# Performance work log

Measured on AMD Instinct MI355X. Metric: run time of the kernel, lower is better.

The kernel has to match this reference:

```python
import jax, jax.numpy as jnp
import numpy as np

NUM_HEADS = 8
NORM_GROUPS = 32
EPS = 1e-5


def setup_inputs() -> dict:
    key = jax.random.key(0)
    k1, k2, k3 = jax.random.split(key, 3)
    b, c, h, w = 16, 256, 64, 64
    x = jax.random.normal(k1, (b, c, h, w), dtype=jnp.float32)
    gn_w = jnp.ones((c,), dtype=jnp.float32)
    gn_b = jnp.zeros((c,), dtype=jnp.float32)
    # 1x1 convs == channel matmuls; init like torch (kaiming-ish scale)
    w_qkv = jax.random.normal(k2, (3 * c, c), dtype=jnp.float32) / np.sqrt(c)
    w_proj = jax.random.normal(k3, (c, c), dtype=jnp.float32) / np.sqrt(c)
    b_proj = jnp.zeros((c,), dtype=jnp.float32)
    return {"x": x, "gn_w": gn_w, "gn_b": gn_b, "w_qkv": w_qkv,
            "w_proj": w_proj, "b_proj": b_proj}


def reference(x, gn_w, gn_b, w_qkv, w_proj, b_proj):
    b, c, h, w = x.shape
    H = NUM_HEADS
    d = c // H
    n = h * w
    # GroupNorm over (channels_per_group, h, w)
    xg = x.reshape(b, NORM_GROUPS, -1)
    mu = jnp.mean(xg, axis=-1, keepdims=True)
    var = jnp.mean(jnp.square(xg - mu), axis=-1, keepdims=True)
    xn = ((xg - mu) * jax.lax.rsqrt(var + EPS)).reshape(b, c, h, w)
    xn = xn * gn_w[None, :, None, None] + gn_b[None, :, None, None]
    # 1x1 conv -> (b, 3c, h, w); channel layout is (qkv, heads, d)
    qkv = jnp.einsum('oc,bchw->bohw', w_qkv, xn)
    qkv = qkv.reshape(b, 3, H, d, n)
    q, k, v = qkv[:, 0], qkv[:, 1], qkv[:, 2]  # each (b, H, d, n)
    k = jax.nn.softmax(k, axis=-1)
    # linear attention: small (d x d) state per head
    att = jnp.einsum('bhdn,bhen->bhde', k, v)
    out = jnp.einsum('bhde,bhdn->bhen', att, q)  # (b, H, d, n)
    out = out.reshape(b, c, h, w)
    return jnp.einsum('oc,bchw->bohw', w_proj, out) + b_proj[None, :, None, None]
```

## Files before the change

kernel.cpp:

```cpp
#include <hip/hip_runtime.h>
#include <stdint.h>

#define BATCH 16
#define CCH   256
#define NSP   4096
#define QKV_M 768

typedef unsigned short u16;
typedef short  short8 __attribute__((ext_vector_type(8)));
typedef float  f32x4  __attribute__((ext_vector_type(4)));

__device__ __forceinline__ float bf2f(u16 h) {
  union { unsigned int u; float f; } x; x.u = ((unsigned int)h) << 16; return x.f;
}
__device__ __forceinline__ u16 f2bf(float f) {
  union { float f; unsigned int u; } x; x.f = f;
  unsigned int r = 0x7fffu + ((x.u >> 16) & 1u);
  return (u16)((x.u + r) >> 16);
}

#define GLB(p) ((__attribute__((address_space(1))) void*)(p))
#define LDSP(p) ((__attribute__((address_space(3))) void*)(p))

__global__ __launch_bounds__(256) void convw_kernel(const float* __restrict__ wq,
                                                    const float* __restrict__ wp,
                                                    u16* __restrict__ dst) {
  const int i = (blockIdx.x * 256 + threadIdx.x) * 4;
  float4 v = (i < 196608) ? *(const float4*)(wq + i)
                          : *(const float4*)(wp + (i - 196608));
  ushort4 o;
  o.x = f2bf(v.x); o.y = f2bf(v.y); o.z = f2bf(v.z); o.w = f2bf(v.w);
  *(ushort4*)(dst + i) = o;
}

__global__ __launch_bounds__(256) void gn_stats(const float* __restrict__ x,
                                                float2* __restrict__ stats,
                                                float* __restrict__ att4) {
  const int blk = blockIdx.x;
  const int tid = threadIdx.x;
  {
    float* az = att4 + (size_t)blk * 264;
    for (int i = tid; i < 264; i += 256) az[i] = 0.f;
  }
  const float4* xv = (const float4*)(x + (size_t)blk * 32768);
  float s = 0.f, ss = 0.f;
  for (int i = tid; i < 8192; i += 256) {
    float4 u = xv[i];
    s  += u.x + u.y + u.z + u.w;
    ss += u.x * u.x + u.y * u.y + u.z * u.z + u.w * u.w;
  }
#pragma unroll
  for (int off = 32; off > 0; off >>= 1) {
    s  += __shfl_down(s, off);
    ss += __shfl_down(ss, off);
  }
  __shared__ float red[8];
  const int wave = tid >> 6, lane = tid & 63;
  if (lane == 0) { red[wave * 2] = s; red[wave * 2 + 1] = ss; }
  __syncthreads();
  if (tid == 0) {
    const float S  = red[0] + red[2] + red[4] + red[6];
    const float SS = red[1] + red[3] + red[5] + red[7];
    const float mean = S * (1.f / 32768.f);
    const float var  = SS * (1.f / 32768.f) - mean * mean;
    stats[blk] = make_float2(mean, rsqrtf(var + 1e-5f));
  }
}

__global__ __launch_bounds__(256) void gn_apply_t(const float* __restrict__ x,
                                                  const float* __restrict__ gw,
                                                  const float* __restrict__ gb,
                                                  const float2* __restrict__ stats,
                                                  u16* __restrict__ xnT) {
  __shared__ u16 ls[64][72];
  const int b = blockIdx.z, c0 = blockIdx.y * 64, n0 = blockIdx.x * 64;
  const int tid = threadIdx.x;
#pragma unroll
  for (int r = 0; r < 4; ++r) {
    const int cc = (tid >> 4) + r * 16;
    const int nn = (tid & 15) * 4;
    const int c = c0 + cc;
    const float2 st = stats[b * 32 + (c >> 3)];
    const float wv = gw[c] * st.y;
    const float bv = gb[c] - st.x * wv;
    float4 u = *(const float4*)(x + ((size_t)b * CCH + c) * NSP + n0 + nn);
    ushort4 o;
    o.x = f2bf(u.x * wv + bv);
    o.y = f2bf(u.y * wv + bv);
    o.z = f2bf(u.z * wv + bv);
    o.w = f2bf(u.w * wv + bv);
    *(ushort4*)&ls[cc][nn] = o;
  }
  __syncthreads();
#pragma unroll
  for (int p = 0; p < 2; ++p) {
    const int idx = tid + p * 256;
    const int nn = idx >> 3;
    const int cb = (idx & 7) * 8;
    u16 tmp[8];
#pragma unroll
    for (int j = 0; j < 8; ++j) tmp[j] = ls[cb + j][nn];
    *(uint4*)(xnT + ((size_t)b * NSP + n0 + nn) * CCH + c0 + cb) = *(uint4*)tmp;
  }
}

template <int OUTF32, int TRQ>
__global__ __launch_bounds__(256) void gemm_mfma(const u16* __restrict__ A,
                                                 const u16* __restrict__ Bt,
                                                 const float* __restrict__ bias,
                                                 void* __restrict__ Cm, int M,
                                                 int aBatch, long btStride) {
  __shared__ __align__(16) u16 smem[17408];
  const int tid = threadIdx.x, wave = tid >> 6, lane = tid & 63;
  const int n0 = blockIdx.x * 128, m0 = blockIdx.y * 128, bz = blockIdx.z;
  const u16* Ab = A + (size_t)bz * aBatch;
  const u16* Bb = Bt + (size_t)bz * btStride;

  const int lrow = lane >> 3;
  const int kcl  = ((lane & 7) ^ lrow) * 8;
  const u16* pA[4]; const u16* pB[4];
#pragma unroll
  for (int j = 0; j < 4; ++j) {
    const int row = j * 32 + wave * 8 + lrow;
    pA[j] = Ab + (size_t)(m0 + row) * CCH + kcl;
    pB[j] = Bb + (size_t)(n0 + row) * CCH + kcl;
  }
  u16* lA = smem;
  u16* lB = smem + 8192;

  const int wm = wave >> 1, wn = wave & 1;
  f32x4 acc[4][4];
#pragma unroll
  for (int i = 0; i < 4; ++i)
#pragma unroll
    for (int j = 0; j < 4; ++j) acc[i][j] = (f32x4){0.f, 0.f, 0.f, 0.f};

  for (int it = 0; it < 4; ++it) {
#pragma unroll
    for (int j = 0; j < 4; ++j) {
      __builtin_amdgcn_global_load_lds(GLB(pA[j]), LDSP(lA + (j * 256 + wave * 64) * 8), 16, 0, 0);
      __builtin_amdgcn_global_load_lds(GLB(pB[j]), LDSP(lB + (j * 256 + wave * 64) * 8), 16, 0, 0);
      pA[j] += 64; pB[j] += 64;
    }
    __syncthreads();
#pragma unroll
    for (int w = 0; w < 2; ++w) {
      const int kcf = w * 4 + (lane >> 4);
      short8 af[4], bfr[4];
#pragma unroll
      for (int mt = 0; mt < 4; ++mt) {
        const int row = wm * 64 + mt * 16 + (lane & 15);
        af[mt] = *(const short8*)&lA[(row * 8 + (kcf ^ (row & 7))) * 8];
      }
#pragma unroll
      for (int nt = 0; nt < 4; ++nt) {
        const int row = wn * 64 + nt * 16 + (lane & 15);
        bfr[nt] = *(const short8*)&lB[(row * 8 + (kcf ^ (row & 7))) * 8];
      }
#pragma unroll
      for (int mt = 0; mt < 4; ++mt)
#pragma unroll
        for (int nt = 0; nt < 4; ++nt)
          acc[mt][nt] = __builtin_amdgcn_mfma_f32_16x16x32_bf16(af[mt], bfr[nt], acc[mt][nt], 0, 0, 0);
    }
    __syncthreads();
  }

  if (!OUTF32) {
    u16* cl = smem;
    const bool tr = TRQ && (m0 < 256);
#pragma unroll
    for (int mt = 0; mt < 4; ++mt)
#pragma unroll
      for (int nt = 0; nt < 4; ++nt)
#pragma unroll
        for (int r = 0; r < 4; ++r) {
          const int row = wm * 64 + mt * 16 + (lane >> 4) * 4 + r;
          const int col = wn * 64 + nt * 16 + (lane & 15);
          if (tr) cl[col * 136 + row] = f2bf(acc[mt][nt][r]);
          else    cl[row * 136 + col] = f2bf(acc[mt][nt][r]);
        }
    __syncthreads();
    u16* C = (u16*)Cm + (size_t)bz * M * NSP;
    if (tr) {
#pragma unroll
      for (int j = 0; j < 8; ++j) {
        const int idx = tid + j * 256;
        const int nl = idx >> 4, mc = (idx & 15) * 8;
        *(uint4*)(C + (size_t)(n0 + nl) * CCH + m0 + mc) =
            *(const uint4*)&cl[nl * 136 + mc];
      }
    } else {
#pragma unroll
      for (int j = 0; j < 8; ++j) {
        const int idx = tid + j * 256;
        const int row = idx >> 4, chunk = idx & 15;
        *(uint4*)(C + (size_t)(m0 + row) * NSP + n0 + chunk * 8) =
            *(const uint4*)&cl[row * 136 + chunk * 8];
      }
    }
  } else {
    float* clf = (float*)smem;
    float* C = (float*)Cm + (size_t)bz * M * NSP;
#pragma unroll
    for (int pass = 0; pass < 2; ++pass) {
      if (wm == pass) {
#pragma unroll
        for (int mt = 0; mt < 4; ++mt)
#pragma unroll
          for (int nt = 0; nt < 4; ++nt)
#pragma unroll
            for (int r = 0; r < 4; ++r) {
              const int rl = mt * 16 + (lane >> 4) * 4 + r;
              const int col = wn * 64 + nt * 16 + (lane & 15);
              clf[rl * 132 + col] = acc[mt][nt][r] + bias[m0 + pass * 64 + rl];
            }
      }
      __syncthreads();
#pragma unroll
      for (int j = 0; j < 8; ++j) {
        const int idx = tid + j * 256;
        const int row = idx >> 5, chunk = idx & 31;
        *(float4*)(C + (size_t)(m0 + pass * 64 + row) * NSP + n0 + chunk * 4) =
            *(const float4*)&clf[row * 132 + chunk * 4];
      }
      __syncthreads();
    }
  }
}

__global__ __launch_bounds__(256) void gemm_kv_att(const u16* __restrict__ A,
                                                   const u16* __restrict__ Bt,
                                                   float* __restrict__ att4) {
  __shared__ __align__(16) u16 smem[34816];
  const int tid = threadIdx.x, wave = tid >> 6, lane = tid & 63;
  const int n0 = blockIdx.x * 128, hg = blockIdx.y, b = blockIdx.z;
  const u16* Bb = Bt + (size_t)b * (size_t)NSP * CCH;

  const int lrow = lane >> 3;
  const int kcl  = ((lane & 7) ^ lrow) * 8;
  u16* lA  = smem;
  u16* lB  = smem + 8192;
  u16* clK = smem + 17408;
  u16* clV = smem;
  const int wm = wave >> 1, wn = wave & 1;

  for (int pass = 0; pass < 2; ++pass) {
    const int m0 = 256 + pass * 256 + hg * 128;
    const u16* pA[4]; const u16* pB[4];
#pragma unroll
    for (int j = 0; j < 4; ++j) {
      const int row = j * 32 + wave * 8 + lrow;
      pA[j] = A  + (size_t)(m0 + row) * CCH + kcl;
      pB[j] = Bb + (size_t)(n0 + row) * CCH + kcl;
    }
    f32x4 acc[4][4];
#pragma unroll
    for (int i = 0; i < 4; ++i)
#pragma unroll
      for (int j = 0; j < 4; ++j) acc[i][j] = (f32x4){0.f, 0.f, 0.f, 0.f};

    for (int it = 0; it < 4; ++it) {
#pragma unroll
      for (int j = 0; j < 4; ++j) {
        __builtin_amdgcn_global_load_lds(GLB(pA[j]), LDSP(lA + (j * 256 + wave * 64) * 8), 16, 0, 0);
        __builtin_amdgcn_global_load_lds(GLB(pB[j]), LDSP(lB + (j * 256 + wave * 64) * 8), 16, 0, 0);
        pA[j] += 64; pB[j] += 64;
      }
      __syncthreads();
#pragma unroll
      for (int w = 0; w < 2; ++w) {
        const int kcf = w * 4 + (lane >> 4);
        short8 af[4], bfr[4];
#pragma unroll
        for (int mt = 0; mt < 4; ++mt) {
          const int row = wm * 64 + mt * 16 + (lane & 15);
          af[mt] = *(const short8*)&lA[(row * 8 + (kcf ^ (row & 7))) * 8];
        }
#pragma unroll
        for (int nt = 0; nt < 4; ++nt) {
          const int row = wn * 64 + nt * 16 + (lane & 15);
          bfr[nt] = *(const short8*)&lB[(row * 8 + (kcf ^ (row & 7))) * 8];
        }
#pragma unroll
        for (int mt = 0; mt < 4; ++mt)
#pragma unroll
          for (int nt = 0; nt < 4; ++nt)
            acc[mt][nt] = __builtin_amdgcn_mfma_f32_16x16x32_bf16(af[mt], bfr[nt], acc[mt][nt], 0, 0, 0);
      }
      __syncthreads();
    }

    u16* cl = pass ? clV : clK;
#pragma unroll
    for (int mt = 0; mt < 4; ++mt)
#pragma unroll
      for (int nt = 0; nt < 4; ++nt)
#pragma unroll
        for (int r = 0; r < 4; ++r) {
          const int row = wm * 64 + mt * 16 + (lane >> 4) * 4 + r;
          const int col = wn * 64 + nt * 16 + (lane & 15);
          const float v = acc[mt][nt][r];
          cl[row * 136 + col] = f2bf(pass ? v : __expf(v));
        }
  }
  __syncthreads();

  const int hh = wave;
  const int bh = b * 8 + hg * 4 + hh;
  f32x4 a2[2][2], al[2];
#pragma unroll
  for (int i = 0; i < 2; ++i) {
    al[i] = (f32x4){0.f, 0.f, 0.f, 0.f};
#pragma unroll
    for (int j = 0; j < 2; ++j) a2[i][j] = (f32x4){0.f, 0.f, 0.f, 0.f};
  }
  short8 ones;
#pragma unroll
  for (int j = 0; j < 8; ++j) ones[j] = (short)0x3F80;

  const int rr = lane & 15, cc8 = (lane >> 4) * 8;
#pragma unroll
  for (int c = 0; c < 4; ++c) {
    const int n = c * 32 + cc8;
    short8 ek0 = *(const short8*)&clK[(hh * 32 + rr) * 136 + n];
    short8 ek1 = *(const short8*)&clK[(hh * 32 + 16 + rr) * 136 + n];
    short8 v0  = *(const short8*)&clV[(hh * 32 + rr) * 136 + n];
    short8 v1  = *(const short8*)&clV[(hh * 32 + 16 + rr) * 136 + n];
    a2[0][0] = __builtin_amdgcn_mfma_f32_16x16x32_bf16(ek0, v0, a2[0][0], 0, 0, 0);
    a2[0][1] = __builtin_amdgcn_mfma_f32_16x16x32_bf16(ek0, v1, a2[0][1], 0, 0, 0);
    a2[1][0] = __builtin_amdgcn_mfma_f32_16x16x32_bf16(ek1, v0, a2[1][0], 0, 0, 0);
    a2[1][1] = __builtin_amdgcn_mfma_f32_16x16x32_bf16(ek1, v1, a2[1][1], 0, 0, 0);
    al[0]    = __builtin_amdgcn_mfma_f32_16x16x32_bf16(ek0, ones, al[0], 0, 0, 0);
    al[1]    = __builtin_amdgcn_mfma_f32_16x16x32_bf16(ek1, ones, al[1], 0, 0, 0);
  }

  float* ap = att4 + (size_t)bh * 1056;
  const int dq = (lane >> 4) * 4;
#pragma unroll
  for (int dh = 0; dh < 2; ++dh) {
#pragma unroll
    for (int eh = 0; eh < 2; ++eh)
#pragma unroll
      for (int j = 0; j < 4; ++j)
        atomicAdd(&ap[(dh * 16 + dq + j) * 32 + eh * 16 + rr], a2[dh][eh][j]);
    if (rr == 0)
#pragma unroll
      for (int j = 0; j < 4; ++j)
        atomicAdd(&ap[1024 + dh * 16 + dq + j], al[dh][j]);
  }
}

__global__ __launch_bounds__(256) void w2_kernel(const u16* __restrict__ wp_bf,
                                                 const float* __restrict__ att4,
                                                 u16* __restrict__ W2) {
  const int b = blockIdx.x >> 4;
  const int o0 = (blockIdx.x & 15) * 16;
  const int tid = threadIdx.x;
  const int h = tid >> 5, d = tid & 31;
  const float* ap = att4 + ((size_t)b * 8 + h) * 1056;
  const float linv = 1.f / ap[1024 + d];
  float as[32];
#pragma unroll
  for (int e = 0; e < 32; ++e) as[e] = ap[d * 32 + e] * linv;
  u16* w2p = W2 + (size_t)b * 65536;
  for (int oi = 0; oi < 16; ++oi) {
    const int o = o0 + oi;
    const uint4* wr = (const uint4*)(wp_bf + o * 256 + h * 32);
    float acc = 0.f;
#pragma unroll
    for (int j = 0; j < 4; ++j) {
      uint4 u = wr[j];
      const u16* w8 = (const u16*)&u;
#pragma unroll
      for (int t = 0; t < 8; ++t) acc += bf2f(w8[t]) * as[j * 8 + t];
    }
    w2p[o * 256 + tid] = f2bf(acc);
  }
}

extern "C" void kernel_launch(void* const* d_in, const int* in_sizes, int n_in,
                              void* d_out, int out_size, void* d_ws, size_t ws_size,
                              hipStream_t stream) {
  const float* x      = (const float*)d_in[0];
  const float* gn_w   = (const float*)d_in[1];
  const float* gn_b   = (const float*)d_in[2];
  const float* w_qkv  = (const float*)d_in[3];
  const float* w_proj = (const float*)d_in[4];
  const float* b_proj = (const float*)d_in[5];
  float* out = (float*)d_out;

  char* ws = (char*)d_ws;
  u16*    xnT   = (u16*)ws;
  u16*    qkv   = (u16*)(ws + 33554432ull);
  float*  att4  = (float*)(ws + 134217728ull);
  float2* stats = (float2*)(ws + 134758400ull);
  u16*    wbf   = (u16*)(ws + 134762496ull);
  u16* wq_bf = wbf;
  u16* wp_bf = wbf + 196608;
  u16* W2 = xnT;

  convw_kernel<<<256, 256, 0, stream>>>(w_qkv, w_proj, wbf);
  gn_stats<<<512, 256, 0, stream>>>(x, stats, att4);
  gn_apply_t<<<dim3(64, 4, 16), 256, 0, stream>>>(x, gn_w, gn_b, stats, xnT);
  gemm_mfma<0, 1><<<dim3(32, 2, 16), 256, 0, stream>>>(wq_bf, xnT, nullptr, qkv,
                                                       QKV_M, 0, (long)NSP * CCH);
  gemm_kv_att<<<dim3(32, 2, 16), 256, 0, stream>>>(wq_bf, xnT, att4);
  w2_kernel<<<256, 256, 0, stream>>>(wp_bf, att4, W2);
  gemm_mfma<1, 0><<<dim3(32, 2, 16), 256, 0, stream>>>(W2, qkv, b_proj, out,
                                                       CCH, 65536, (long)QKV_M * NSP);
}
```

Baseline: 246.9 us.

## Fold query projection into output weights and drop QKV materialization

```diff
diff --git a/kernel.cpp b/kernel.cpp
--- a/kernel.cpp
+++ b/kernel.cpp
@@ -4,7 +4,6 @@
 #define BATCH 16
 #define CCH   256
 #define NSP   4096
-#define QKV_M 768
 
 typedef unsigned short u16;
 typedef short  short8 __attribute__((ext_vector_type(8)));
@@ -31,6 +30,27 @@
   ushort4 o;
   o.x = f2bf(v.x); o.y = f2bf(v.y); o.z = f2bf(v.z); o.w = f2bf(v.w);
   *(ushort4*)(dst + i) = o;
+}
+
+__global__ __launch_bounds__(256) void wqt_kernel(const u16* __restrict__ wq_bf,
+                                                  u16* __restrict__ wqT) {
+  __shared__ u16 ls[64][72];
+  const int r0 = blockIdx.y * 64, c0 = blockIdx.x * 64;
+  const int t = threadIdx.x;
+#pragma unroll
+  for (int j = 0; j < 2; ++j) {
+    const int row = j * 32 + (t >> 3), col8 = (t & 7) * 8;
+    *(uint4*)&ls[row][col8] = *(const uint4*)(wq_bf + (r0 + row) * 256 + c0 + col8);
+  }
+  __syncthreads();
+#pragma unroll
+  for (int j = 0; j < 2; ++j) {
+    const int crow = j * 32 + (t >> 3), d8 = (t & 7) * 8;
+    u16 tmp[8];
+#pragma unroll
+    for (int k = 0; k < 8; ++k) tmp[k] = ls[d8 + k][crow];
+    *(uint4*)(wqT + (c0 + crow) * 256 + r0 + d8) = *(uint4*)tmp;
+  }
 }
 
 __global__ __launch_bounds__(256) void gn_stats(const float* __restrict__ x,
@@ -104,12 +124,12 @@
   }
 }
 
-template <int OUTF32, int TRQ>
+template <int OUTF32>
 __global__ __launch_bounds__(256) void gemm_mfma(const u16* __restrict__ A,
                                                  const u16* __restrict__ Bt,
                                                  const float* __restrict__ bias,
                                                  void* __restrict__ Cm, int M,
-                                                 int aBatch, long btStride) {
+                                                 int aBatch, long btStride, int ldc) {
   __shared__ __align__(16) u16 smem[17408];
   const int tid = threadIdx.x, wave = tid >> 6, lane = tid & 63;
   const int n0 = blockIdx.x * 128, m0 = blockIdx.y * 128, bz = blockIdx.z;
@@ -168,7 +188,6 @@
 
   if (!OUTF32) {
     u16* cl = smem;
-    const bool tr = TRQ && (m0 < 256);
 #pragma unroll
     for (int mt = 0; mt < 4; ++mt)
 #pragma unroll
@@ -177,31 +196,20 @@
         for (int r = 0; r < 4; ++r) {
           const int row = wm * 64 + mt * 16 + (lane >> 4) * 4 + r;
           const int col = wn * 64 + nt * 16 + (lane & 15);
-          if (tr) cl[col * 136 + row] = f2bf(acc[mt][nt][r]);
-          else    cl[row * 136 + col] = f2bf(acc[mt][nt][r]);
+          cl[row * 136 + col] = f2bf(acc[mt][nt][r]);
         }
     __syncthreads();
-    u16* C = (u16*)Cm + (size_t)bz * M * NSP;
-    if (tr) {
-#pragma unroll
-      for (int j = 0; j < 8; ++j) {
-        const int idx = tid + j * 256;
-        const int nl = idx >> 4, mc = (idx & 15) * 8;
-        *(uint4*)(C + (size_t)(n0 + nl) * CCH + m0 + mc) =
-            *(const uint4*)&cl[nl * 136 + mc];
-      }
-    } else {
-#pragma unroll
-      for (int j = 0; j < 8; ++j) {
-        const int idx = tid + j * 256;
-        const int row = idx >> 4, chunk = idx & 15;
-        *(uint4*)(C + (size_t)(m0 + row) * NSP + n0 + chunk * 8) =
-            *(const uint4*)&cl[row * 136 + chunk * 8];
-      }
+    u16* C = (u16*)Cm + (size_t)bz * (size_t)M * ldc;
+#pragma unroll
+    for (int j = 0; j < 8; ++j) {
+      const int idx = tid + j * 256;
+      const int row = idx >> 4, chunk = idx & 15;
+      *(uint4*)(C + (size_t)(m0 + row) * ldc + n0 + chunk * 8) =
+          *(const uint4*)&cl[row * 136 + chunk * 8];
     }
   } else {
     float* clf = (float*)smem;
-    float* C = (float*)Cm + (size_t)bz * M * NSP;
+    float* C = (float*)Cm + (size_t)bz * (size_t)M * ldc;
 #pragma unroll
     for (int pass = 0; pass < 2; ++pass) {
       if (wm == pass) {
@@ -221,7 +229,7 @@
       for (int j = 0; j < 8; ++j) {
         const int idx = tid + j * 256;
         const int row = idx >> 5, chunk = idx & 31;
-        *(float4*)(C + (size_t)(m0 + pass * 64 + row) * NSP + n0 + chunk * 4) =
+        *(float4*)(C + (size_t)(m0 + pass * 64 + row) * ldc + n0 + chunk * 4) =
             *(const float4*)&clf[row * 132 + chunk * 4];
       }
       __syncthreads();
@@ -232,7 +240,7 @@
 __global__ __launch_bounds__(256) void gemm_kv_att(const u16* __restrict__ A,
                                                    const u16* __restrict__ Bt,
                                                    float* __restrict__ att4) {
-  __shared__ __align__(16) u16 smem[34816];
+  __shared__ __align__(16) u16 smem[20992];
   const int tid = threadIdx.x, wave = tid >> 6, lane = tid & 63;
   const int n0 = blockIdx.x * 128, hg = blockIdx.y, b = blockIdx.z;
   const u16* Bb = Bt + (size_t)b * (size_t)NSP * CCH;
@@ -240,41 +248,46 @@
   const int lrow = lane >> 3;
   const int kcl  = ((lane & 7) ^ lrow) * 8;
   u16* lA  = smem;
-  u16* lB  = smem + 8192;
-  u16* clK = smem + 17408;
+  u16* lB  = smem + 4096;
   u16* clV = smem;
+  u16* clK = smem + 12288;
   const int wm = wave >> 1, wn = wave & 1;
 
   for (int pass = 0; pass < 2; ++pass) {
-    const int m0 = 256 + pass * 256 + hg * 128;
-    const u16* pA[4]; const u16* pB[4];
-#pragma unroll
-    for (int j = 0; j < 4; ++j) {
-      const int row = j * 32 + wave * 8 + lrow;
-      pA[j] = A  + (size_t)(m0 + row) * CCH + kcl;
-      pB[j] = Bb + (size_t)(n0 + row) * CCH + kcl;
-    }
-    f32x4 acc[4][4];
-#pragma unroll
-    for (int i = 0; i < 4; ++i)
+    const int m0 = 256 + pass * 256 + hg * 64;
+    const u16* pA[2]; const u16* pB[4];
+#pragma unroll
+    for (int j = 0; j < 2; ++j)
+      pA[j] = A + (size_t)(m0 + j * 32 + wave * 8 + lrow) * CCH + kcl;
+#pragma unroll
+    for (int j = 0; j < 4; ++j)
+      pB[j] = Bb + (size_t)(n0 + j * 32 + wave * 8 + lrow) * CCH + kcl;
+
+    f32x4 acc[2][4];
+#pragma unroll
+    for (int i = 0; i < 2; ++i)
 #pragma unroll
       for (int j = 0; j < 4; ++j) acc[i][j] = (f32x4){0.f, 0.f, 0.f, 0.f};
 
     for (int it = 0; it < 4; ++it) {
 #pragma unroll
+      for (int j = 0; j < 2; ++j) {
+        __builtin_amdgcn_global_load_lds(GLB(pA[j]), LDSP(lA + (j * 256 + wave * 64) * 8), 16, 0, 0);
+        pA[j] += 64;
+      }
+#pragma unroll
       for (int j = 0; j < 4; ++j) {
-        __builtin_amdgcn_global_load_lds(GLB(pA[j]), LDSP(lA + (j * 256 + wave * 64) * 8), 16, 0, 0);
         __builtin_amdgcn_global_load_lds(GLB(pB[j]), LDSP(lB + (j * 256 + wave * 64) * 8), 16, 0, 0);
-        pA[j] += 64; pB[j] += 64;
+        pB[j] += 64;
       }
       __syncthreads();
 #pragma unroll
       for (int w = 0; w < 2; ++w) {
         const int kcf = w * 4 + (lane >> 4);
-        short8 af[4], bfr[4];
-#pragma unroll
-        for (int mt = 0; mt < 4; ++mt) {
-          const int row = wm * 64 + mt * 16 + (lane & 15);
+        short8 af[2], bfr[4];
+#pragma unroll
+        for (int mt = 0; mt < 2; ++mt) {
+          const int row = wm * 32 + mt * 16 + (lane & 15);
           af[mt] = *(const short8*)&lA[(row * 8 + (kcf ^ (row & 7))) * 8];
         }
 #pragma unroll
@@ -283,7 +296,7 @@
           bfr[nt] = *(const short8*)&lB[(row * 8 + (kcf ^ (row & 7))) * 8];
         }
 #pragma unroll
-        for (int mt = 0; mt < 4; ++mt)
+        for (int mt = 0; mt < 2; ++mt)
 #pragma unroll
           for (int nt = 0; nt < 4; ++nt)
             acc[mt][nt] = __builtin_amdgcn_mfma_f32_16x16x32_bf16(af[mt], bfr[nt], acc[mt][nt], 0, 0, 0);
@@ -293,12 +306,12 @@
 
     u16* cl = pass ? clV : clK;
 #pragma unroll
-    for (int mt = 0; mt < 4; ++mt)
+    for (int mt = 0; mt < 2; ++mt)
 #pragma unroll
       for (int nt = 0; nt < 4; ++nt)
 #pragma unroll
         for (int r = 0; r < 4; ++r) {
-          const int row = wm * 64 + mt * 16 + (lane >> 4) * 4 + r;
+          const int row = wm * 32 + mt * 16 + (lane >> 4) * 4 + r;
           const int col = wn * 64 + nt * 16 + (lane & 15);
           const float v = acc[mt][nt][r];
           cl[row * 136 + col] = f2bf(pass ? v : __expf(v));
@@ -306,8 +319,8 @@
   }
   __syncthreads();
 
-  const int hh = wave;
-  const int bh = b * 8 + hg * 4 + hh;
+  const int hh = wave >> 1, nhalf = wave & 1;
+  const int bh = b * 8 + hg * 2 + hh;
   f32x4 a2[2][2], al[2];
 #pragma unroll
   for (int i = 0; i < 2; ++i) {
@@ -321,8 +334,8 @@
 
   const int rr = lane & 15, cc8 = (lane >> 4) * 8;
 #pragma unroll
-  for (int c = 0; c < 4; ++c) {
-    const int n = c * 32 + cc8;
+  for (int c = 0; c < 2; ++c) {
+    const int n = (nhalf * 2 + c) * 32 + cc8;
     short8 ek0 = *(const short8*)&clK[(hh * 32 + rr) * 136 + n];
     short8 ek1 = *(const short8*)&clK[(hh * 32 + 16 + rr) * 136 + n];
     short8 v0  = *(const short8*)&clV[(hh * 32 + rr) * 136 + n];
@@ -334,20 +347,43 @@
     al[0]    = __builtin_amdgcn_mfma_f32_16x16x32_bf16(ek0, ones, al[0], 0, 0, 0);
     al[1]    = __builtin_amdgcn_mfma_f32_16x16x32_bf16(ek1, ones, al[1], 0, 0, 0);
   }
-
-  float* ap = att4 + (size_t)bh * 1056;
+  __syncthreads();
+
+  float* red  = (float*)smem;
+  float* redl = red + 2176;
   const int dq = (lane >> 4) * 4;
-#pragma unroll
-  for (int dh = 0; dh < 2; ++dh) {
-#pragma unroll
-    for (int eh = 0; eh < 2; ++eh)
-#pragma unroll
-      for (int j = 0; j < 4; ++j)
-        atomicAdd(&ap[(dh * 16 + dq + j) * 32 + eh * 16 + rr], a2[dh][eh][j]);
-    if (rr == 0)
-#pragma unroll
-      for (int j = 0; j < 4; ++j)
-        atomicAdd(&ap[1024 + dh * 16 + dq + j], al[dh][j]);
+  if (nhalf == 1) {
+#pragma unroll
+    for (int dh = 0; dh < 2; ++dh) {
+#pragma unroll
+      for (int eh = 0; eh < 2; ++eh)
+#pragma unroll
+        for (int j = 0; j < 4; ++j)
+          red[hh * 1088 + (dh * 16 + dq + j) * 34 + eh * 16 + rr] = a2[dh][eh][j];
+      if (rr == 0)
+#pragma unroll
+        for (int j = 0; j < 4; ++j) redl[hh * 32 + dh * 16 + dq + j] = al[dh][j];
+    }
+  }
+  __syncthreads();
+  if (nhalf == 0) {
+    float* ap = att4 + (size_t)bh * 1056;
+#pragma unroll
+    for (int dh = 0; dh < 2; ++dh) {
+#pragma unroll
+      for (int eh = 0; eh < 2; ++eh)
+#pragma unroll
+        for (int j = 0; j < 4; ++j) {
+          const int d = dh * 16 + dq + j, e = eh * 16 + rr;
+          atomicAdd(&ap[d * 32 + e], a2[dh][eh][j] + red[hh * 1088 + d * 34 + e]);
+        }
+      if (rr == 0)
+#pragma unroll
+        for (int j = 0; j < 4; ++j) {
+          const int d = dh * 16 + dq + j;
+          atomicAdd(&ap[1024 + d], al[dh][j] + redl[hh * 32 + d]);
+        }
+    }
   }
 }
 
@@ -392,21 +428,23 @@
 
   char* ws = (char*)d_ws;
   u16*    xnT   = (u16*)ws;
-  u16*    qkv   = (u16*)(ws + 33554432ull);
-  float*  att4  = (float*)(ws + 134217728ull);
-  float2* stats = (float2*)(ws + 134758400ull);
-  u16*    wbf   = (u16*)(ws + 134762496ull);
+  u16*    wbf   = (u16*)(ws + 33554432ull);
+  u16*    wqT   = (u16*)(ws + 34078720ull);
+  u16*    W2    = (u16*)(ws + 34209792ull);
+  u16*    W3    = (u16*)(ws + 36306944ull);
+  float*  att4  = (float*)(ws + 38404096ull);
+  float2* stats = (float2*)(ws + 38944768ull);
   u16* wq_bf = wbf;
   u16* wp_bf = wbf + 196608;
-  u16* W2 = xnT;
 
   convw_kernel<<<256, 256, 0, stream>>>(w_qkv, w_proj, wbf);
+  wqt_kernel<<<dim3(4, 4), 256, 0, stream>>>(wq_bf, wqT);
   gn_stats<<<512, 256, 0, stream>>>(x, stats, att4);
   gn_apply_t<<<dim3(64, 4, 16), 256, 0, stream>>>(x, gn_w, gn_b, stats, xnT);
-  gemm_mfma<0, 1><<<dim3(32, 2, 16), 256, 0, stream>>>(wq_bf, xnT, nullptr, qkv,
-                                                       QKV_M, 0, (long)NSP * CCH);
-  gemm_kv_att<<<dim3(32, 2, 16), 256, 0, stream>>>(wq_bf, xnT, att4);
+  gemm_kv_att<<<dim3(32, 4, 16), 256, 0, stream>>>(wq_bf, xnT, att4);
   w2_kernel<<<256, 256, 0, stream>>>(wp_bf, att4, W2);
-  gemm_mfma<1, 0><<<dim3(32, 2, 16), 256, 0, stream>>>(W2, qkv, b_proj, out,
-                                                       CCH, 65536, (long)QKV_M * NSP);
-}
+  gemm_mfma<0><<<dim3(2, 2, 16), 256, 0, stream>>>(W2, wqT, nullptr, W3,
+                                                   CCH, 65536, 0L, CCH);
+  gemm_mfma<1><<<dim3(32, 2, 16), 256, 0, stream>>>(W3, xnT, b_proj, out,
+                                                    CCH, 65536, (long)NSP * CCH, NSP);
+}
```

Measured after the change: 223.5 us. 9.5% less time.
